# Kernel tuning notes

Measured on AMD Instinct MI355X. Metric: run time of the kernel, lower is better.

## Reference

```python
import jax, jax.numpy as jnp
import numpy as np

ALPHA = 0.2       # LeakyReLU negative slope
ADJ_THRE = 0.0
NEG_INF = -1e30   # finite stand-in for -inf (safe in fp32 softmax)


def setup_inputs() -> dict:
    key = jax.random.key(0)
    k1, k2, k3, k4, k5, k6 = jax.random.split(key, 6)
    b, n_k = 4, 512
    in_f, e_in_f, out_f = 256, 64, 256
    x = jax.random.normal(k1, (b, n_k, in_f), dtype=jnp.float32)
    edge = jax.random.normal(k2, (b, n_k, n_k, e_in_f), dtype=jnp.float32)
    adj = jax.random.uniform(k3, (b, n_k, n_k), dtype=jnp.float32)
    # xavier_uniform with gain=1.414
    def xavier(k, shape, gain=1.414):
        fan_in, fan_out = shape[0], shape[1]
        bound = gain * np.sqrt(6.0 / (fan_in + fan_out))
        return jax.random.uniform(k, shape, dtype=jnp.float32, minval=-bound, maxval=bound)
    W = xavier(k4, (in_f, out_f))
    W1 = xavier(k5, (e_in_f, out_f))
    a = xavier(k6, (3 * out_f, 1))
    return {"x": x, "edge": edge, "adj": adj, "W": W, "W1": W1, "a": a}


def reference(x, edge, adj, W, W1, a):
    # x:(b,n,in_f) edge:(b,n,n,e_in) adj:(b,n,n)
    out_f = W.shape[1]
    h = jnp.matmul(x, W)                      # (b, n, o)
    a1 = a[:out_f, 0]                         # score weight for h_i (row)
    a2 = a[out_f:2 * out_f, 0]                # score weight for h_j (col)
    a3 = a[2 * out_f:, 0]                     # score weight for edge proj
    # concat([h_i, h_j, e_h]) @ a == h_i@a1 + h_j@a2 + (edge@W1)@a3
    s_i = jnp.einsum('bno,o->bn', h, a1)      # (b, n)
    s_j = jnp.einsum('bno,o->bn', h, a2)      # (b, n)
    w1a3 = W1 @ a3                            # (e_in,) fused: edge@(W1@a3)
    s_e = jnp.einsum('bije,e->bij', edge, w1a3)  # (b, n, n)
    e = jax.nn.leaky_relu(s_i[:, :, None] + s_j[:, None, :] + s_e, ALPHA)
    e = jnp.where(adj > ADJ_THRE, e, NEG_INF)
    attention = jax.nn.softmax(e, axis=2)     # (b, n, n); dropout off (eval)
    h_prime = jnp.matmul(attention, h)        # (b, n, o)
    return jax.nn.elu(h_prime)                # concat=True
```

## Files before the change

### kernel.cpp

```cpp
#include <hip/hip_runtime.h>
#include <cstdint>
#include <cstddef>

#define ALPHA 0.2f
#define NEG_INF -1e30f

constexpr int B = 4, N = 512, IN_F = 256, E_F = 64, OUT_F = 256;

__global__ __launch_bounds__(256) void k_h(const float* __restrict__ x,
                                           const float* __restrict__ W,
                                           const float* __restrict__ W1,
                                           const float* __restrict__ a,
                                           float* __restrict__ h,
                                           float* __restrict__ s_i,
                                           float* __restrict__ s_j,
                                           float* __restrict__ w1a3) {
    int tid = threadIdx.x;
    if (blockIdx.x == (B * N) / 4) {
        int e = tid >> 2, part = tid & 3;
        const float* row = W1 + (size_t)e * OUT_F + part * 64;
        const float* a3 = a + 2 * OUT_F + part * 64;
        float s = 0.f;
        #pragma unroll 8
        for (int o = 0; o < 64; ++o) s += row[o] * a3[o];
        s += __shfl_xor(s, 1);
        s += __shfl_xor(s, 2);
        if (part == 0) w1a3[e] = s;
        return;
    }
    int wv = tid >> 6, lane = tid & 63;
    int row = blockIdx.x * 4 + wv;
    int c4 = lane * 4;

    __shared__ float xs[4][IN_F];
    *(float4*)&xs[wv][c4] = *(const float4*)&x[(size_t)row * IN_F + c4];
    __syncthreads();

    float4 acc = {0.f, 0.f, 0.f, 0.f};
    for (int k = 0; k < IN_F; ++k) {
        float4 w4 = *(const float4*)&W[(size_t)k * OUT_F + c4];
        float xv = xs[wv][k];
        acc.x = fmaf(xv, w4.x, acc.x);
        acc.y = fmaf(xv, w4.y, acc.y);
        acc.z = fmaf(xv, w4.z, acc.z);
        acc.w = fmaf(xv, w4.w, acc.w);
    }
    *(float4*)&h[(size_t)row * OUT_F + c4] = acc;

    float4 a1v = *(const float4*)&a[c4];
    float4 a2v = *(const float4*)&a[OUT_F + c4];
    float p1 = acc.x * a1v.x + acc.y * a1v.y + acc.z * a1v.z + acc.w * a1v.w;
    float p2 = acc.x * a2v.x + acc.y * a2v.y + acc.z * a2v.z + acc.w * a2v.w;
    #pragma unroll
    for (int off = 32; off; off >>= 1) {
        p1 += __shfl_xor(p1, off);
        p2 += __shfl_xor(p2, off);
    }
    if (lane == 0) { s_i[row] = p1; s_j[row] = p2; }
}

__global__ __launch_bounds__(256) void k_att_out(const float* __restrict__ edge,
                                                 const float* __restrict__ adj,
                                                 const float* __restrict__ s_i,
                                                 const float* __restrict__ s_j,
                                                 const float* __restrict__ w1a3,
                                                 const float* __restrict__ h,
                                                 float* __restrict__ out) {
    int bi = blockIdx.x;
    int b = bi >> 9;
    int tid = threadIdx.x;
    int wv = tid >> 6, lane = tid & 63;

    __shared__ __align__(16) float part[N][17];
    __shared__ float sjs[N];
    __shared__ float adjs[N];
    __shared__ __align__(16) float w1a3s[E_F];
    __shared__ float redm[4], reds[4];

    if (tid < E_F) w1a3s[tid] = w1a3[tid];
    sjs[tid]        = s_j[b * N + tid];
    sjs[tid + 256]  = s_j[b * N + tid + 256];
    adjs[tid]       = adj[(size_t)bi * N + tid];
    adjs[tid + 256] = adj[(size_t)bi * N + tid + 256];
    float si = s_i[bi];
    __syncthreads();

    int col = lane & 15;
    int jg  = lane >> 4;
    float4 w4 = *(const float4*)&w1a3s[col * 4];
    const float* ebase = edge + (size_t)bi * N * E_F;

    #pragma unroll
    for (int it = 0; it < 8; ++it) {
        int jw = it * 64 + wv * 16;
        #pragma unroll
        for (int i = 0; i < 4; ++i) {
            int j = jw + i * 4 + jg;
            float4 ev = *(const float4*)(ebase + (size_t)j * E_F + col * 4);
            part[j][col] = ev.x * w4.x + ev.y * w4.y + ev.z * w4.z + ev.w * w4.w;
        }
    }
    __syncthreads();

    float v0 = si + sjs[tid];
    float v1 = si + sjs[tid + 256];
    #pragma unroll
    for (int c = 0; c < 16; ++c) {
        v0 += part[tid][c];
        v1 += part[tid + 256][c];
    }
    v0 = v0 > 0.f ? v0 : ALPHA * v0;
    v1 = v1 > 0.f ? v1 : ALPHA * v1;
    v0 = (adjs[tid] > 0.f) ? v0 : NEG_INF;
    v1 = (adjs[tid + 256] > 0.f) ? v1 : NEG_INF;

    float m = fmaxf(v0, v1);
    #pragma unroll
    for (int off = 32; off; off >>= 1) m = fmaxf(m, __shfl_xor(m, off));
    if (lane == 0) redm[wv] = m;
    __syncthreads();
    m = fmaxf(fmaxf(redm[0], redm[1]), fmaxf(redm[2], redm[3]));

    float e0 = __expf(v0 - m);
    float e1 = __expf(v1 - m);
    float s = e0 + e1;
    #pragma unroll
    for (int off = 32; off; off >>= 1) s += __shfl_xor(s, off);
    if (lane == 0) reds[wv] = s;
    __syncthreads();
    s = reds[0] + reds[1] + reds[2] + reds[3];
    float inv = 1.f / s;

    sjs[tid]       = e0 * inv;
    sjs[tid + 256] = e1 * inv;
    __syncthreads();

    const float* hb = h + (size_t)b * N * OUT_F;
    int c4 = lane * 4;
    float4 acc = {0.f, 0.f, 0.f, 0.f};
    int k0 = wv * 128;
    for (int k = k0; k < k0 + 128; ++k) {
        float av = sjs[k];
        float4 hv = *(const float4*)&hb[(size_t)k * OUT_F + c4];
        acc.x = fmaf(av, hv.x, acc.x);
        acc.y = fmaf(av, hv.y, acc.y);
        acc.z = fmaf(av, hv.z, acc.z);
        acc.w = fmaf(av, hv.w, acc.w);
    }
    float* flat = &part[0][0];
    ((float4*)(flat + wv * 256))[lane] = acc;
    __syncthreads();
    float r = flat[tid] + flat[256 + tid] + flat[512 + tid] + flat[768 + tid];
    out[(size_t)bi * OUT_F + tid] = r > 0.f ? r : (expf(r) - 1.f);
}

extern "C" void kernel_launch(void* const* d_in, const int* in_sizes, int n_in,
                              void* d_out, int out_size, void* d_ws, size_t ws_size,
                              hipStream_t stream) {
    const float* x    = (const float*)d_in[0];
    const float* edge = (const float*)d_in[1];
    const float* adj  = (const float*)d_in[2];
    const float* W    = (const float*)d_in[3];
    const float* W1   = (const float*)d_in[4];
    const float* a    = (const float*)d_in[5];
    float* out = (float*)d_out;

    float* ws = (float*)d_ws;
    float* h_buf    = ws;
    float* si_buf   = h_buf + (size_t)B * N * OUT_F;
    float* sj_buf   = si_buf + B * N;
    float* w1a3_buf = sj_buf + B * N;

    k_h<<<(B * N) / 4 + 1, 256, 0, stream>>>(x, W, W1, a, h_buf, si_buf, sj_buf, w1a3_buf);
    k_att_out<<<B * N, 256, 0, stream>>>(edge, adj, si_buf, sj_buf, w1a3_buf, h_buf, out);
}
```

Before: 409.5 us.

## Process four attention rows per block to reuse h loads

The attention kernel now gives each block four consecutive query rows instead of one. Each row's edge-score softmax is computed in turn and stored in shared memory, and the four rows then share a single pass over h, accumulating four outputs per loaded h vector. This cuts h reads from L2/global memory by four. In exchange the grid has a quarter as many blocks, shared memory use per block rises, and each block runs the four edge-projection phases one after another with extra barriers.

Result: no change. 409.8 us (+0.1%).

```diff
diff --git a/kernel.cpp b/kernel.cpp
--- a/kernel.cpp
+++ b/kernel.cpp
@@ -66,12 +66,13 @@
                                                  const float* __restrict__ w1a3,
                                                  const float* __restrict__ h,
                                                  float* __restrict__ out) {
-    int bi = blockIdx.x;
-    int b = bi >> 9;
+    int bi0 = blockIdx.x * 4;
+    int b = bi0 >> 9;
     int tid = threadIdx.x;
     int wv = tid >> 6, lane = tid & 63;
 
     __shared__ __align__(16) float part[N][17];
+    __shared__ __align__(16) float attL[4][N];
     __shared__ float sjs[N];
     __shared__ float adjs[N];
     __shared__ __align__(16) float w1a3s[E_F];
@@ -80,78 +81,105 @@
     if (tid < E_F) w1a3s[tid] = w1a3[tid];
     sjs[tid]        = s_j[b * N + tid];
     sjs[tid + 256]  = s_j[b * N + tid + 256];
-    adjs[tid]       = adj[(size_t)bi * N + tid];
-    adjs[tid + 256] = adj[(size_t)bi * N + tid + 256];
-    float si = s_i[bi];
+    float si0 = s_i[bi0], si1 = s_i[bi0 + 1], si2 = s_i[bi0 + 2], si3 = s_i[bi0 + 3];
     __syncthreads();
 
     int col = lane & 15;
     int jg  = lane >> 4;
     float4 w4 = *(const float4*)&w1a3s[col * 4];
-    const float* ebase = edge + (size_t)bi * N * E_F;
 
     #pragma unroll
-    for (int it = 0; it < 8; ++it) {
-        int jw = it * 64 + wv * 16;
-        #pragma unroll
-        for (int i = 0; i < 4; ++i) {
-            int j = jw + i * 4 + jg;
-            float4 ev = *(const float4*)(ebase + (size_t)j * E_F + col * 4);
-            part[j][col] = ev.x * w4.x + ev.y * w4.y + ev.z * w4.z + ev.w * w4.w;
+    for (int r = 0; r < 4; ++r) {
+        int bi = bi0 + r;
+        float si = (r == 0) ? si0 : (r == 1) ? si1 : (r == 2) ? si2 : si3;
+        adjs[tid]       = adj[(size_t)bi * N + tid];
+        adjs[tid + 256] = adj[(size_t)bi * N + tid + 256];
+
+        const float* ebase = edge + (size_t)bi * N * E_F;
+        #pragma unroll
+        for (int it = 0; it < 8; ++it) {
+            int jw = it * 64 + wv * 16;
+            #pragma unroll
+            for (int i = 0; i < 4; ++i) {
+                int j = jw + i * 4 + jg;
+                float4 ev = *(const float4*)(ebase + (size_t)j * E_F + col * 4);
+                part[j][col] = ev.x * w4.x + ev.y * w4.y + ev.z * w4.z + ev.w * w4.w;
+            }
         }
-    }
-    __syncthreads();
-
-    float v0 = si + sjs[tid];
-    float v1 = si + sjs[tid + 256];
-    #pragma unroll
-    for (int c = 0; c < 16; ++c) {
-        v0 += part[tid][c];
-        v1 += part[tid + 256][c];
-    }
-    v0 = v0 > 0.f ? v0 : ALPHA * v0;
-    v1 = v1 > 0.f ? v1 : ALPHA * v1;
-    v0 = (adjs[tid] > 0.f) ? v0 : NEG_INF;
-    v1 = (adjs[tid + 256] > 0.f) ? v1 : NEG_INF;
-
-    float m = fmaxf(v0, v1);
-    #pragma unroll
-    for (int off = 32; off; off >>= 1) m = fmaxf(m, __shfl_xor(m, off));
-    if (lane == 0) redm[wv] = m;
-    __syncthreads();
-    m = fmaxf(fmaxf(redm[0], redm[1]), fmaxf(redm[2], redm[3]));
-
-    float e0 = __expf(v0 - m);
-    float e1 = __expf(v1 - m);
-    float s = e0 + e1;
-    #pragma unroll
-    for (int off = 32; off; off >>= 1) s += __shfl_xor(s, off);
-    if (lane == 0) reds[wv] = s;
-    __syncthreads();
-    s = reds[0] + reds[1] + reds[2] + reds[3];
-    float inv = 1.f / s;
-
-    sjs[tid]       = e0 * inv;
-    sjs[tid + 256] = e1 * inv;
-    __syncthreads();
+        __syncthreads();
+
+        float v0 = si + sjs[tid];
+        float v1 = si + sjs[tid + 256];
+        #pragma unroll
+        for (int c = 0; c < 16; ++c) {
+            v0 += part[tid][c];
+            v1 += part[tid + 256][c];
+        }
+        v0 = v0 > 0.f ? v0 : ALPHA * v0;
+        v1 = v1 > 0.f ? v1 : ALPHA * v1;
+        v0 = (adjs[tid] > 0.f) ? v0 : NEG_INF;
+        v1 = (adjs[tid + 256] > 0.f) ? v1 : NEG_INF;
+
+        float m = fmaxf(v0, v1);
+        #pragma unroll
+        for (int off = 32; off; off >>= 1) m = fmaxf(m, __shfl_xor(m, off));
+        if (lane == 0) redm[wv] = m;
+        __syncthreads();
+        m = fmaxf(fmaxf(redm[0], redm[1]), fmaxf(redm[2], redm[3]));
+
+        float e0 = __expf(v0 - m);
+        float e1 = __expf(v1 - m);
+        float s = e0 + e1;
+        #pragma unroll
+        for (int off = 32; off; off >>= 1) s += __shfl_xor(s, off);
+        if (lane == 0) reds[wv] = s;
+        __syncthreads();
+        s = reds[0] + reds[1] + reds[2] + reds[3];
+        float inv = 1.f / s;
+
+        attL[r][tid]       = e0 * inv;
+        attL[r][tid + 256] = e1 * inv;
+        __syncthreads();
+    }
 
     const float* hb = h + (size_t)b * N * OUT_F;
     int c4 = lane * 4;
-    float4 acc = {0.f, 0.f, 0.f, 0.f};
+    float4 ac0 = {0,0,0,0}, ac1 = {0,0,0,0}, ac2 = {0,0,0,0}, ac3 = {0,0,0,0};
     int k0 = wv * 128;
-    for (int k = k0; k < k0 + 128; ++k) {
-        float av = sjs[k];
-        float4 hv = *(const float4*)&hb[(size_t)k * OUT_F + c4];
-        acc.x = fmaf(av, hv.x, acc.x);
-        acc.y = fmaf(av, hv.y, acc.y);
-        acc.z = fmaf(av, hv.z, acc.z);
-        acc.w = fmaf(av, hv.w, acc.w);
+    for (int k = k0; k < k0 + 128; k += 4) {
+        float4 a0 = *(const float4*)&attL[0][k];
+        float4 a1 = *(const float4*)&attL[1][k];
+        float4 a2 = *(const float4*)&attL[2][k];
+        float4 a3 = *(const float4*)&attL[3][k];
+        #pragma unroll
+        for (int q = 0; q < 4; ++q) {
+            float4 hv = *(const float4*)&hb[(size_t)(k + q) * OUT_F + c4];
+            float f0 = q == 0 ? a0.x : q == 1 ? a0.y : q == 2 ? a0.z : a0.w;
+            float f1 = q == 0 ? a1.x : q == 1 ? a1.y : q == 2 ? a1.z : a1.w;
+            float f2 = q == 0 ? a2.x : q == 1 ? a2.y : q == 2 ? a2.z : a2.w;
+            float f3 = q == 0 ? a3.x : q == 1 ? a3.y : q == 2 ? a3.z : a3.w;
+            ac0.x = fmaf(f0, hv.x, ac0.x); ac0.y = fmaf(f0, hv.y, ac0.y);
+            ac0.z = fmaf(f0, hv.z, ac0.z); ac0.w = fmaf(f0, hv.w, ac0.w);
+            ac1.x = fmaf(f1, hv.x, ac1.x); ac1.y = fmaf(f1, hv.y, ac1.y);
+            ac1.z = fmaf(f1, hv.z, ac1.z); ac1.w = fmaf(f1, hv.w, ac1.w);
+            ac2.x = fmaf(f2, hv.x, ac2.x); ac2.y = fmaf(f2, hv.y, ac2.y);
+            ac2.z = fmaf(f2, hv.z, ac2.z); ac2.w = fmaf(f2, hv.w, ac2.w);
+            ac3.x = fmaf(f3, hv.x, ac3.x); ac3.y = fmaf(f3, hv.y, ac3.y);
+            ac3.z = fmaf(f3, hv.z, ac3.z); ac3.w = fmaf(f3, hv.w, ac3.w);
+        }
     }
     float* flat = &part[0][0];
-    ((float4*)(flat + wv * 256))[lane] = acc;
+    *(float4*)(flat + wv * 1024 +   0 + c4) = ac0;
+    *(float4*)(flat + wv * 1024 + 256 + c4) = ac1;
+    *(float4*)(flat + wv * 1024 + 512 + c4) = ac2;
+    *(float4*)(flat + wv * 1024 + 768 + c4) = ac3;
     __syncthreads();
-    float r = flat[tid] + flat[256 + tid] + flat[512 + tid] + flat[768 + tid];
-    out[(size_t)bi * OUT_F + tid] = r > 0.f ? r : (expf(r) - 1.f);
+    #pragma unroll
+    for (int r = 0; r < 4; ++r) {
+        float v = flat[r * 256 + tid] + flat[1024 + r * 256 + tid]
+                + flat[2048 + r * 256 + tid] + flat[3072 + r * 256 + tid];
+        out[(size_t)(bi0 + r) * OUT_F + tid] = v > 0.f ? v : (expf(v) - 1.f);
+    }
 }
 
 extern "C" void kernel_launch(void* const* d_in, const int* in_sizes, int n_in,
@@ -172,5 +200,5 @@
     float* w1a3_buf = sj_buf + B * N;
 
     k_h<<<(B * N) / 4 + 1, 256, 0, stream>>>(x, W, W1, a, h_buf, si_buf, sj_buf, w1a3_buf);
-    k_att_out<<<B * N, 256, 0, stream>>>(edge, adj, si_buf, sj_buf, w1a3_buf, h_buf, out);
+    k_att_out<<<(B * N) / 4, 256, 0, stream>>>(edge, adj, si_buf, sj_buf, w1a3_buf, h_buf, out);
 }
```
